# Kernel tuning notes

Hardware: AMD Instinct MI355X
Metric: run time of the kernel (lower is better)

Reference implementation:

```python
import jax, jax.numpy as jnp
import numpy as np

N_NODES = 49984   # 32 graphs x 1562 nodes
N_EDGES = 799744  # avg degree 16
DIM_IN = 64
WIDTH = 256
DEPTH = 3         # depth+1 = 4 GCNConv blocks
N_GRAPHS = 32
NODES_PER_GRAPH = 1562


def setup_inputs() -> dict:
    key = jax.random.key(0)
    ks = jax.random.split(key, 12)
    nb = DEPTH + 1
    s_f = 1.0 / np.sqrt(DIM_IN)
    s_g = 1.0 / np.sqrt(WIDTH)
    return {
        "x": jax.random.normal(ks[0], (N_NODES, DIM_IN), dtype=jnp.float32),
        "edge_index": jax.random.randint(ks[1], (2, N_EDGES), 0, N_NODES, dtype=jnp.int32),
        "center": jax.random.randint(ks[2], (N_GRAPHS,), 0, NODES_PER_GRAPH, dtype=jnp.int32),
        "ptr": jnp.arange(N_GRAPHS + 1, dtype=jnp.int32) * NODES_PER_GRAPH,
        # foot: Conv1d(dim_input, width, 1) == per-node linear
        "Wf": jax.random.uniform(ks[3], (WIDTH, DIM_IN), jnp.float32, -s_f, s_f),
        "bf": jax.random.uniform(ks[4], (WIDTH,), jnp.float32, -s_f, s_f),
        # stacked GCNConv params: weight [nb, width, width] (in->out), bias [nb, width]
        "Wg": jax.random.uniform(ks[5], (nb, WIDTH, WIDTH), jnp.float32, -s_g, s_g),
        "bg": jax.random.uniform(ks[6], (nb, WIDTH), jnp.float32, -s_g, s_g),
        # head: Conv1d(width, 7, 1)
        "Wh": jax.random.uniform(ks[7], (7, WIDTH), jnp.float32, -s_g, s_g),
        "bh": jax.random.uniform(ks[8], (7,), jnp.float32, -s_g, s_g),
    }


def reference(x, edge_index, center, ptr, Wf, bf, Wg, bg, Wh, bh):
    N = x.shape[0]
    # foot: 1x1 conv (per-node linear) + exact GELU; dropout = identity (eval)
    h = jax.nn.gelu(x @ Wf.T + bf, approximate=False)  # [N, W]

    # gcn_norm with self-loops (same for every layer since edges are static)
    loops = jnp.arange(N, dtype=edge_index.dtype)
    row = jnp.concatenate([edge_index[0], loops])  # source
    col = jnp.concatenate([edge_index[1], loops])  # target
    deg = jax.ops.segment_sum(jnp.ones_like(row, dtype=h.dtype), col, num_segments=N)
    dis = jnp.where(deg > 0, jax.lax.rsqrt(jnp.maximum(deg, 1.0)), 0.0)
    norm = dis[row] * dis[col]  # [E+N]

    for l in range(Wg.shape[0]):
        xl = h @ Wg[l]                                   # [N, W] linear transform
        msg = xl[row] * norm[:, None]                    # gather + edge scale
        agg = jax.ops.segment_sum(msg, col, num_segments=N) + bg[l]
        h = h + agg                                      # residual

    out = jax.nn.gelu(h, approximate=False) @ Wh.T + bh  # [N, 7]
    return out[center + ptr[:-1]]                        # [B, 7]
```

## Files before the change

kernel.cpp:

```cpp
#include <hip/hip_runtime.h>
#include <math.h>

#define WIDTH 256
typedef unsigned short u16;
typedef unsigned int u32;
typedef __attribute__((ext_vector_type(4))) float f32x4;
typedef __attribute__((ext_vector_type(8))) short bf16x8;

__device__ __forceinline__ float gelu_exact(float v) {
    return 0.5f * v * (1.0f + erff(v * 0.70710678118654752f));
}
__device__ __forceinline__ u16 f2b(float x) {
    u32 u = __builtin_bit_cast(u32, x);
    return (u16)((u + 0x7fffu + ((u >> 16) & 1u)) >> 16);
}
__device__ __forceinline__ float b2f_lo(u32 v) {
    return __builtin_bit_cast(float, v << 16);
}
__device__ __forceinline__ float b2f_hi(u32 v) {
    return __builtin_bit_cast(float, v & 0xffff0000u);
}
__device__ __forceinline__ float b2fu(u16 b) {
    return __builtin_bit_cast(float, ((u32)b) << 16);
}
__device__ __forceinline__ u32 pack2(float a, float b) {
    return (u32)f2b(a) | ((u32)f2b(b) << 16);
}

#define PREP_WG   (4 * 65536)
#define PREP_WF   (256 * 64)
__global__ void k_prep(const float* __restrict__ Wg, const float* __restrict__ Wf,
                       const float* __restrict__ x,
                       u16* __restrict__ WgT, u16* __restrict__ WfT,
                       u16* __restrict__ xb, int total8) {
    int idx = blockIdx.x * blockDim.x + threadIdx.x;
    if (idx < PREP_WG) {
        int l = idx >> 16;
        int k = (idx >> 8) & 255;
        int n = idx & 255;
        WgT[(size_t)l * 65536 + (size_t)n * 256 + k] = f2b(Wg[idx]);
    } else if (idx < PREP_WG + PREP_WF) {
        int j = idx - PREP_WG;
        WfT[j] = f2b(Wf[j]);
    } else if (idx < PREP_WG + PREP_WF + total8) {
        int i = idx - (PREP_WG + PREP_WF);
        const float4 v0 = *reinterpret_cast<const float4*>(&x[(size_t)i * 8]);
        const float4 v1 = *reinterpret_cast<const float4*>(&x[(size_t)i * 8 + 4]);
        uint4 o;
        o.x = pack2(v0.x, v0.y);
        o.y = pack2(v0.z, v0.w);
        o.z = pack2(v1.x, v1.y);
        o.w = pack2(v1.z, v1.w);
        *reinterpret_cast<uint4*>(&xb[(size_t)i * 8]) = o;
    }
}

__global__ void k_hist(const int* __restrict__ col, int* __restrict__ deg,
                       u16* __restrict__ rank, int E) {
    int i = blockIdx.x * blockDim.x + threadIdx.x;
    if (i < E) rank[i] = (u16)atomicAdd(&deg[col[i]], 1);
}

__global__ __launch_bounds__(256) void k_scan1(const int* __restrict__ deg, int* __restrict__ off,
                                               int* __restrict__ part, float* __restrict__ dis, int N) {
    __shared__ int buf[256];
    const int t = threadIdx.x;
    const int gid = blockIdx.x * 256 + t;
    const int v = (gid < N) ? deg[gid] : 0;
    if (gid < N) dis[gid] = rsqrtf(1.0f + (float)v);
    buf[t] = v;
    __syncthreads();
#pragma unroll
    for (int d = 1; d < 256; d <<= 1) {
        int add = (t >= d) ? buf[t - d] : 0;
        __syncthreads();
        buf[t] += add;
        __syncthreads();
    }
    if (gid < N) off[gid] = buf[t] - v;
    if (t == 255) part[blockIdx.x] = buf[255];
}

__global__ __launch_bounds__(256) void k_scan3(int* __restrict__ off, const int* __restrict__ part,
                                               int NB, int N, int E) {
    __shared__ int buf[256];
    const int t = threadIdx.x;
    int v = (t < NB) ? part[t] : 0;
    buf[t] = v;
    __syncthreads();
#pragma unroll
    for (int d = 1; d < 256; d <<= 1) {
        int add = (t >= d) ? buf[t - d] : 0;
        __syncthreads();
        buf[t] += add;
        __syncthreads();
    }
    const int base = (blockIdx.x == 0) ? 0 : buf[blockIdx.x - 1];
    const int gid = blockIdx.x * 256 + t;
    if (gid < N) off[gid] += base;
    if (gid == 0) off[N] = E;
}

__global__ void k_fill(const int* __restrict__ row, const int* __restrict__ col,
                       const u16* __restrict__ rank, const float* __restrict__ dis,
                       const int* __restrict__ off, u32* __restrict__ csr, int E) {
    int i = blockIdx.x * blockDim.x + threadIdx.x;
    if (i < E) {
        const int r = row[i];
        const int pos = off[col[i]] + (int)rank[i];
        csr[pos] = (u32)(u16)r | ((u32)f2b(dis[r]) << 16);
    }
}

__global__ void k_front(const int* __restrict__ center, const int* __restrict__ ptr,
                        const int* __restrict__ off, const u32* __restrict__ csr,
                        int* __restrict__ flags, int* __restrict__ list, int* __restrict__ cnt) {
    const int g = blockIdx.x;
    const int node = center[g] + ptr[g];
    const int t = threadIdx.x;
    const int e0 = off[node];
    const int e1 = off[node + 1];
    if (t == 0) {
        if (atomicExch(&flags[node], 1) == 0) list[atomicAdd(cnt, 1)] = node;
    }
    for (int e = e0 + t; e < e1; e += 256) {
        const int s = (int)(csr[e] & 0xffffu);
        if (atomicExch(&flags[s], 1) == 0) list[atomicAdd(cnt, 1)] = s;
    }
}

__global__ void k_front2(const int* __restrict__ off, const u32* __restrict__ csr,
                         const int* __restrict__ list1, const int* __restrict__ cnt1,
                         int* __restrict__ flags2, int* __restrict__ list2, int* __restrict__ cnt2) {
    const int n1 = cnt1[0];
    const int t = threadIdx.x;
    for (int idx = blockIdx.x; idx < n1; idx += gridDim.x) {
        const int node = list1[idx];
        if (t == 0) {
            if (atomicExch(&flags2[node], 1) == 0) list2[atomicAdd(cnt2, 1)] = node;
        }
        const int e0 = off[node];
        const int e1 = off[node + 1];
        for (int e = e0 + t; e < e1; e += 256) {
            const int s = (int)(csr[e] & 0xffffu);
            if (atomicExch(&flags2[s], 1) == 0) list2[atomicAdd(cnt2, 1)] = s;
        }
    }
}

template <int KDIM, bool FOOT>
__global__ __launch_bounds__(512) void k_gemm_mfma(const u16* __restrict__ A,
                                                   const u16* __restrict__ BT,
                                                   const float* __restrict__ bias,
                                                   u16* __restrict__ Cb,
                                                   float* __restrict__ Cf, int nrows) {
    __shared__ u16 As[128 * 64];
    __shared__ u16 Bs[256 * 64];

    const int tid = threadIdx.x;
    const int w = tid >> 6;
    const int l = tid & 63;
    const int m0 = blockIdx.x * 128;
    const int wr = w >> 2;
    const int wc = w & 3;

    const int lr = l >> 3;
    const int lc = l & 7;
    const int src_slot = lc ^ lr;

    f32x4 acc[4][4] = {};

#pragma unroll
    for (int ks = 0; ks < KDIM / 64; ++ks) {
        const int k0 = ks * 64;
#pragma unroll
        for (int i = 0; i < 2; ++i) {
            const u16* asrc = A + (size_t)(m0 + 16 * w + 8 * i + lr) * KDIM + k0 + src_slot * 8;
            __builtin_amdgcn_global_load_lds(
                (const __attribute__((address_space(1))) u32*)asrc,
                (__attribute__((address_space(3))) u32*)(As + (16 * w + 8 * i) * 64), 16, 0, 0);
        }
#pragma unroll
        for (int j = 0; j < 4; ++j) {
            const u16* bsrc = BT + (size_t)(32 * w + 8 * j + lr) * KDIM + k0 + src_slot * 8;
            __builtin_amdgcn_global_load_lds(
                (const __attribute__((address_space(1))) u32*)bsrc,
                (__attribute__((address_space(3))) u32*)(Bs + (32 * w + 8 * j) * 64), 16, 0, 0);
        }
        asm volatile("s_waitcnt vmcnt(0)" ::: "memory");
        __syncthreads();

        bf16x8 a[4][2], b[4][2];
#pragma unroll
        for (int fr = 0; fr < 4; ++fr) {
            const int row = 64 * wr + fr * 16 + (l & 15);
#pragma unroll
            for (int kk = 0; kk < 2; ++kk)
                a[fr][kk] = *reinterpret_cast<const bf16x8*>(
                    &As[row * 64 + ((kk * 4 + (l >> 4)) ^ (row & 7)) * 8]);
        }
#pragma unroll
        for (int fc = 0; fc < 4; ++fc) {
            const int row = 64 * wc + fc * 16 + (l & 15);
#pragma unroll
            for (int kk = 0; kk < 2; ++kk)
                b[fc][kk] = *reinterpret_cast<const bf16x8*>(
                    &Bs[row * 64 + ((kk * 4 + (l >> 4)) ^ (row & 7)) * 8]);
        }
#pragma unroll
        for (int fr = 0; fr < 4; ++fr)
#pragma unroll
            for (int fc = 0; fc < 4; ++fc) {
                acc[fr][fc] = __builtin_amdgcn_mfma_f32_16x16x32_bf16(a[fr][0], b[fc][0], acc[fr][fc], 0, 0, 0);
                acc[fr][fc] = __builtin_amdgcn_mfma_f32_16x16x32_bf16(a[fr][1], b[fc][1], acc[fr][fc], 0, 0, 0);
            }
        __syncthreads();
    }

    const int r0 = (l >> 4) * 4;
    const int ci = l & 15;
#pragma unroll
    for (int fr = 0; fr < 4; ++fr)
#pragma unroll
        for (int fc = 0; fc < 4; ++fc) {
            const int col = 64 * wc + fc * 16 + ci;
#pragma unroll
            for (int r = 0; r < 4; ++r) {
                const int row = m0 + 64 * wr + fr * 16 + r0 + r;
                if (row < nrows) {
                    const size_t p = (size_t)row * WIDTH + col;
                    if (FOOT) {
                        const float o = gelu_exact(acc[fr][fc][r] + bias[col]);
                        Cf[p] = o;
                        Cb[p] = f2b(o);
                    } else {
                        Cb[p] = f2b(acc[fr][fc][r]);
                    }
                }
            }
        }
}

#define EDGE_FMA(vv, dd_)                          \
    acc[0] = fmaf(dd_, b2f_lo(vv.x), acc[0]);      \
    acc[1] = fmaf(dd_, b2f_hi(vv.x), acc[1]);      \
    acc[2] = fmaf(dd_, b2f_lo(vv.y), acc[2]);      \
    acc[3] = fmaf(dd_, b2f_hi(vv.y), acc[3]);

__device__ __forceinline__ void agg_node_body(const int* __restrict__ off,
                                              const u32* __restrict__ csr,
                                              const float* __restrict__ dis,
                                              const u16* __restrict__ xlb,
                                              const float* __restrict__ bg,
                                              float* __restrict__ h,
                                              u16* __restrict__ hb,
                                              int node, int hl, int ch0) {
    const int c = ch0 + hl * 4;
    const int e0 = off[node];
    const int e1 = off[node + 1];
    const float di = dis[node];

    float acc[4];
    {
        const uint2 v = *reinterpret_cast<const uint2*>(&xlb[(size_t)node * WIDTH + c]);
        acc[0] = di * b2f_lo(v.x);
        acc[1] = di * b2f_hi(v.x);
        acc[2] = di * b2f_lo(v.y);
        acc[3] = di * b2f_hi(v.y);
    }

    for (int base = e0; base < e1; base += 32) {
        const int m = min(32, e1 - base);
        u32 ep = 0;
        if (hl < m) ep = csr[base + hl];
        int j = 0;
        for (; j + 8 <= m; j += 8) {
            uint2 vv[8];
            float dd[8];
#pragma unroll
            for (int q = 0; q < 8; ++q) {
                const u32 e = (u32)__shfl((int)ep, j + q, 32);
                dd[q] = b2f_hi(e);
                vv[q] = *reinterpret_cast<const uint2*>(&xlb[(size_t)(e & 0xffffu) * WIDTH + c]);
            }
#pragma unroll
            for (int q = 0; q < 8; ++q) { EDGE_FMA(vv[q], dd[q]) }
        }
        if (j + 4 <= m) {
            uint2 vv[4];
            float dd[4];
#pragma unroll
            for (int q = 0; q < 4; ++q) {
                const u32 e = (u32)__shfl((int)ep, j + q, 32);
                dd[q] = b2f_hi(e);
                vv[q] = *reinterpret_cast<const uint2*>(&xlb[(size_t)(e & 0xffffu) * WIDTH + c]);
            }
#pragma unroll
            for (int q = 0; q < 4; ++q) { EDGE_FMA(vv[q], dd[q]) }
            j += 4;
        }
        for (; j < m; ++j) {
            const u32 e = (u32)__shfl((int)ep, j, 32);
            const float dj = b2f_hi(e);
            const uint2 v = *reinterpret_cast<const uint2*>(&xlb[(size_t)(e & 0xffffu) * WIDTH + c]);
            EDGE_FMA(v, dj)
        }
    }

    const size_t p = (size_t)node * WIDTH + c;
    const float4 hv = *reinterpret_cast<const float4*>(&h[p]);
    const float4 bv = *reinterpret_cast<const float4*>(&bg[c]);
    const float o0 = hv.x + bv.x + di * acc[0];
    const float o1 = hv.y + bv.y + di * acc[1];
    const float o2 = hv.z + bv.z + di * acc[2];
    const float o3 = hv.w + bv.w + di * acc[3];
    float4 w0;
    w0.x = o0; w0.y = o1; w0.z = o2; w0.w = o3;
    *reinterpret_cast<float4*>(&h[p]) = w0;
    uint2 ob;
    ob.x = pack2(o0, o1);
    ob.y = pack2(o2, o3);
    *reinterpret_cast<uint2*>(&hb[p]) = ob;
}

__global__ __launch_bounds__(256) void k_agg(const int* __restrict__ off,
                                             const u32* __restrict__ csr,
                                             const float* __restrict__ dis,
                                             const u16* __restrict__ xlb,
                                             const float* __restrict__ bg,
                                             float* __restrict__ h,
                                             u16* __restrict__ hb, int nbh, int N) {
    int bh = blockIdx.x;
    int ch0 = 0;
    if (bh >= nbh) { ch0 = 128; bh -= nbh; }
    const int node = (bh * 256 + threadIdx.x) >> 5;
    if (node >= N) return;
    agg_node_body(off, csr, dis, xlb, bg, h, hb, node, threadIdx.x & 31, ch0);
}

__global__ __launch_bounds__(256) void k_agg_list(const int* __restrict__ off,
                                                  const u32* __restrict__ csr,
                                                  const float* __restrict__ dis,
                                                  const u16* __restrict__ xlb,
                                                  const float* __restrict__ bg,
                                                  float* __restrict__ h,
                                                  u16* __restrict__ hb,
                                                  const int* __restrict__ list,
                                                  const int* __restrict__ cnt) {
    const int nitems = cnt[0] * 2;
    const int hl = threadIdx.x & 31;
    const int stride = (gridDim.x * 256) >> 5;
    for (int item = (blockIdx.x * 256 + threadIdx.x) >> 5; item < nitems; item += stride) {
        const int node = list[item >> 1];
        const int ch0 = (item & 1) << 7;
        agg_node_body(off, csr, dis, xlb, bg, h, hb, node, hl, ch0);
    }
}
#undef EDGE_FMA

__global__ __launch_bounds__(256) void k_tail(const int* __restrict__ off,
                                              const u32* __restrict__ csr,
                                              const float* __restrict__ dis,
                                              const u16* __restrict__ hb,
                                              const float* __restrict__ h,
                                              const float* __restrict__ Wg3,
                                              const float* __restrict__ bg3,
                                              const float* __restrict__ Wh,
                                              const float* __restrict__ bh,
                                              const int* __restrict__ center,
                                              const int* __restrict__ ptr,
                                              float* __restrict__ out) {
    __shared__ float aggK[256];
    __shared__ u32 es[256];
    __shared__ float gs[256];
    const int g = blockIdx.x;
    const int t = threadIdx.x;
    const int node = center[g] + ptr[g];
    const int e0 = off[node];
    const int e1 = off[node + 1];
    const float di = dis[node];

    float acc = di * b2fu(hb[(size_t)node * WIDTH + t]);
    for (int base = e0; base < e1; base += 256) {
        const int m = min(256, e1 - base);
        if (t < m) es[t] = csr[base + t];
        __syncthreads();
        int j = 0;
        for (; j + 4 <= m; j += 4) {
            const u32 a0 = es[j + 0], a1 = es[j + 1], a2 = es[j + 2], a3 = es[j + 3];
            const float v0 = b2fu(hb[(size_t)(a0 & 0xffffu) * WIDTH + t]);
            const float v1 = b2fu(hb[(size_t)(a1 & 0xffffu) * WIDTH + t]);
            const float v2 = b2fu(hb[(size_t)(a2 & 0xffffu) * WIDTH + t]);
            const float v3 = b2fu(hb[(size_t)(a3 & 0xffffu) * WIDTH + t]);
            acc = fmaf(b2f_hi(a0), v0, acc);
            acc = fmaf(b2f_hi(a1), v1, acc);
            acc = fmaf(b2f_hi(a2), v2, acc);
            acc = fmaf(b2f_hi(a3), v3, acc);
        }
        for (; j < m; ++j) {
            const u32 a = es[j];
            acc = fmaf(b2f_hi(a), b2fu(hb[(size_t)(a & 0xffffu) * WIDTH + t]), acc);
        }
        __syncthreads();
    }
    aggK[t] = acc;
    __syncthreads();

    float mv = 0.0f;
#pragma unroll 8
    for (int k = 0; k < 256; ++k)
        mv = fmaf(aggK[k], Wg3[(size_t)k * 256 + t], mv);
    const float h4 = h[(size_t)node * WIDTH + t] + bg3[t] + di * mv;
    gs[t] = gelu_exact(h4);
    __syncthreads();
    if (t < 7) {
        float o = bh[t];
        for (int k = 0; k < 256; ++k)
            o = fmaf(gs[k], Wh[t * 256 + k], o);
        out[g * 7 + t] = o;
    }
}

extern "C" void kernel_launch(void* const* d_in, const int* in_sizes, int n_in,
                              void* d_out, int out_size, void* d_ws, size_t ws_size,
                              hipStream_t stream) {
    const float* x      = (const float*)d_in[0];
    const int*   ei     = (const int*)d_in[1];
    const int*   center = (const int*)d_in[2];
    const int*   ptr    = (const int*)d_in[3];
    const float* Wf     = (const float*)d_in[4];
    const float* bf     = (const float*)d_in[5];
    const float* Wg     = (const float*)d_in[6];
    const float* bg     = (const float*)d_in[7];
    const float* Wh     = (const float*)d_in[8];
    const float* bh     = (const float*)d_in[9];

    const int E = in_sizes[1] / 2;
    const int N = in_sizes[0] / 64;
    const int B = in_sizes[2];

    char* ws = (char*)d_ws;
    size_t o = 0;
    float* h       = (float*)(ws + o); o += (size_t)N * WIDTH * 4;
    u16*   hb      = (u16*)  (ws + o); o += (size_t)N * WIDTH * 2;
    u16*   xlb     = (u16*)  (ws + o); o += (size_t)N * WIDTH * 2;
    u16*   xb      = (u16*)  (ws + o); o += (size_t)N * 64 * 2;
    float* dis     = (float*)(ws + o); o += (size_t)N * 4;
    int*   deg     = (int*)  (ws + o); o += (size_t)N * 4;
    int*   off     = (int*)  (ws + o); o += (size_t)(N + 1) * 4;
    int*   part    = (int*)  (ws + o); o += 1024;
    u16*   rank    = (u16*)  (ws + o); o += (size_t)E * 2;
    u32*   csr     = (u32*)  (ws + o); o += (size_t)E * 4;
    u16*   WgT     = (u16*)  (ws + o); o += (size_t)4 * 65536 * 2;
    u16*   WfT     = (u16*)  (ws + o); o += (size_t)256 * 64 * 2;
    int*   flags   = (int*)  (ws + o); o += (size_t)N * 4;
    int*   flags2  = (int*)  (ws + o); o += (size_t)N * 4;
    int*   cnt     = (int*)  (ws + o); o += 128;
    int*   cnt2    = (int*)  (ws + o); o += 128;
    int*   list1   = (int*)  (ws + o); o += (size_t)N * 4;
    int*   list2   = (int*)  (ws + o); o += (size_t)N * 4;

    const int* rowv = ei;
    const int* colv = ei + E;

    const int nb = (N + 255) / 256;
    const int eb = (E + 255) / 256;

    hipMemsetAsync(deg, 0, (size_t)N * 4, stream);
    hipMemsetAsync(flags, 0, (size_t)N * 8 + 256, stream);
    const int total8 = N * 64 / 8;
    const int prep_threads = PREP_WG + PREP_WF + total8;
    k_prep<<<(prep_threads + 255) / 256, 256, 0, stream>>>(Wg, Wf, x, WgT, WfT, xb, total8);
    k_hist<<<eb, 256, 0, stream>>>(colv, deg, rank, E);
    k_scan1<<<nb, 256, 0, stream>>>(deg, off, part, dis, N);
    k_scan3<<<nb, 256, 0, stream>>>(off, part, nb, N, E);
    k_fill<<<eb, 256, 0, stream>>>(rowv, colv, rank, dis, off, csr, E);
    k_front<<<B, 256, 0, stream>>>(center, ptr, off, csr, flags, list1, cnt);
    k_front2<<<64, 256, 0, stream>>>(off, csr, list1, cnt, flags2, list2, cnt2);

    const int gb = (N + 127) / 128;
    k_gemm_mfma<64, true><<<gb, 512, 0, stream>>>(xb, WfT, bf, hb, h, N);

    const int nbh = N / 8;
    k_gemm_mfma<256, false><<<gb, 512, 0, stream>>>(hb, WgT, nullptr, xlb, nullptr, N);
    k_agg<<<2 * nbh, 256, 0, stream>>>(off, csr, dis, xlb, bg, h, hb, nbh, N);

    k_gemm_mfma<256, false><<<gb, 512, 0, stream>>>(hb, WgT + (size_t)1 * 65536, nullptr, xlb, nullptr, N);
    k_agg_list<<<1024, 256, 0, stream>>>(off, csr, dis, xlb, bg + (size_t)1 * WIDTH, h, hb, list2, cnt2);

    k_gemm_mfma<256, false><<<gb, 512, 0, stream>>>(hb, WgT + (size_t)2 * 65536, nullptr, xlb, nullptr, N);
    k_agg_list<<<256, 256, 0, stream>>>(off, csr, dis, xlb, bg + (size_t)2 * WIDTH, h, hb, list1, cnt);

    k_tail<<<B, 256, 0, stream>>>(off, csr, dis, hb, h,
                                  Wg + (size_t)3 * 65536, bg + (size_t)3 * WIDTH,
                                  Wh, bh, center, ptr, (float*)d_out);
}
```

Baseline: 273.3 us.

## Restrict layer-3 GEMM to gathered frontier rows and split degree histogram atomics

```diff
diff --git a/kernel.cpp b/kernel.cpp
--- a/kernel.cpp
+++ b/kernel.cpp
@@ -55,29 +55,42 @@
     }
 }
 
-__global__ void k_hist(const int* __restrict__ col, int* __restrict__ deg,
-                       u16* __restrict__ rank, int E) {
+__global__ void k_hist8(const int* __restrict__ col, int* __restrict__ deg8,
+                        u16* __restrict__ rank, int E, int N) {
     int i = blockIdx.x * blockDim.x + threadIdx.x;
-    if (i < E) rank[i] = (u16)atomicAdd(&deg[col[i]], 1);
-}
-
-__global__ __launch_bounds__(256) void k_scan1(const int* __restrict__ deg, int* __restrict__ off,
-                                               int* __restrict__ part, float* __restrict__ dis, int N) {
+    if (i < E) {
+        const int c = blockIdx.x & 7;
+        rank[i] = (u16)atomicAdd(&deg8[(size_t)c * N + col[i]], 1);
+    }
+}
+
+__global__ __launch_bounds__(256) void k_scan1(const int* __restrict__ deg8, int* __restrict__ off,
+                                               int* __restrict__ part, float* __restrict__ dis,
+                                               u16* __restrict__ base8, int N) {
     __shared__ int buf[256];
     const int t = threadIdx.x;
     const int gid = blockIdx.x * 256 + t;
-    const int v = (gid < N) ? deg[gid] : 0;
-    if (gid < N) dis[gid] = rsqrtf(1.0f + (float)v);
-    buf[t] = v;
+    int d = 0;
+    if (gid < N) {
+        int run = 0;
+#pragma unroll
+        for (int c = 0; c < 8; ++c) {
+            base8[(size_t)c * N + gid] = (u16)run;
+            run += deg8[(size_t)c * N + gid];
+        }
+        d = run;
+        dis[gid] = rsqrtf(1.0f + (float)run);
+    }
+    buf[t] = d;
     __syncthreads();
 #pragma unroll
-    for (int d = 1; d < 256; d <<= 1) {
-        int add = (t >= d) ? buf[t - d] : 0;
+    for (int dd = 1; dd < 256; dd <<= 1) {
+        int add = (t >= dd) ? buf[t - dd] : 0;
         __syncthreads();
         buf[t] += add;
         __syncthreads();
     }
-    if (gid < N) off[gid] = buf[t] - v;
+    if (gid < N) off[gid] = buf[t] - d;
     if (t == 255) part[blockIdx.x] = buf[255];
 }
 
@@ -102,12 +115,15 @@
 }
 
 __global__ void k_fill(const int* __restrict__ row, const int* __restrict__ col,
-                       const u16* __restrict__ rank, const float* __restrict__ dis,
-                       const int* __restrict__ off, u32* __restrict__ csr, int E) {
+                       const u16* __restrict__ rank, const u16* __restrict__ base8,
+                       const float* __restrict__ dis,
+                       const int* __restrict__ off, u32* __restrict__ csr, int E, int N) {
     int i = blockIdx.x * blockDim.x + threadIdx.x;
     if (i < E) {
+        const int c = blockIdx.x & 7;
         const int r = row[i];
-        const int pos = off[col[i]] + (int)rank[i];
+        const int cc = col[i];
+        const int pos = off[cc] + (int)base8[(size_t)c * N + cc] + (int)rank[i];
         csr[pos] = (u32)(u16)r | ((u32)f2b(dis[r]) << 16);
     }
 }
@@ -239,6 +255,94 @@
                 }
             }
         }
+}
+
+__global__ __launch_bounds__(512) void k_gemm_gather(const u16* __restrict__ A,
+                                                     const u16* __restrict__ BT,
+                                                     u16* __restrict__ Cb,
+                                                     const int* __restrict__ list,
+                                                     const int* __restrict__ cnt) {
+    __shared__ u16 As[128 * 64];
+    __shared__ u16 Bs[256 * 64];
+
+    const int nrows = cnt[0];
+    const int tid = threadIdx.x;
+    const int w = tid >> 6;
+    const int l = tid & 63;
+    const int wr = w >> 2;
+    const int wc = w & 3;
+
+    const int lr = l >> 3;
+    const int lc = l & 7;
+    const int src_slot = lc ^ lr;
+
+    for (int m0 = blockIdx.x * 128; m0 < nrows; m0 += gridDim.x * 128) {
+        f32x4 acc[4][4] = {};
+
+#pragma unroll
+        for (int ks = 0; ks < 4; ++ks) {
+            const int k0 = ks * 64;
+#pragma unroll
+            for (int i = 0; i < 2; ++i) {
+                int ridx = m0 + 16 * w + 8 * i + lr;
+                ridx = min(ridx, nrows - 1);
+                const u16* asrc = A + (size_t)list[ridx] * WIDTH + k0 + src_slot * 8;
+                __builtin_amdgcn_global_load_lds(
+                    (const __attribute__((address_space(1))) u32*)asrc,
+                    (__attribute__((address_space(3))) u32*)(As + (16 * w + 8 * i) * 64), 16, 0, 0);
+            }
+#pragma unroll
+            for (int j = 0; j < 4; ++j) {
+                const u16* bsrc = BT + (size_t)(32 * w + 8 * j + lr) * WIDTH + k0 + src_slot * 8;
+                __builtin_amdgcn_global_load_lds(
+                    (const __attribute__((address_space(1))) u32*)bsrc,
+                    (__attribute__((address_space(3))) u32*)(Bs + (32 * w + 8 * j) * 64), 16, 0, 0);
+            }
+            asm volatile("s_waitcnt vmcnt(0)" ::: "memory");
+            __syncthreads();
+
+            bf16x8 a[4][2], b[4][2];
+#pragma unroll
+            for (int fr = 0; fr < 4; ++fr) {
+                const int row = 64 * wr + fr * 16 + (l & 15);
+#pragma unroll
+                for (int kk = 0; kk < 2; ++kk)
+                    a[fr][kk] = *reinterpret_cast<const bf16x8*>(
+                        &As[row * 64 + ((kk * 4 + (l >> 4)) ^ (row & 7)) * 8]);
+            }
+#pragma unroll
+            for (int fc = 0; fc < 4; ++fc) {
+                const int row = 64 * wc + fc * 16 + (l & 15);
+#pragma unroll
+                for (int kk = 0; kk < 2; ++kk)
+                    b[fc][kk] = *reinterpret_cast<const bf16x8*>(
+                        &Bs[row * 64 + ((kk * 4 + (l >> 4)) ^ (row & 7)) * 8]);
+            }
+#pragma unroll
+            for (int fr = 0; fr < 4; ++fr)
+#pragma unroll
+                for (int fc = 0; fc < 4; ++fc) {
+                    acc[fr][fc] = __builtin_amdgcn_mfma_f32_16x16x32_bf16(a[fr][0], b[fc][0], acc[fr][fc], 0, 0, 0);
+                    acc[fr][fc] = __builtin_amdgcn_mfma_f32_16x16x32_bf16(a[fr][1], b[fc][1], acc[fr][fc], 0, 0, 0);
+                }
+            __syncthreads();
+        }
+
+        const int r0 = (l >> 4) * 4;
+        const int ci = l & 15;
+#pragma unroll
+        for (int fr = 0; fr < 4; ++fr)
+#pragma unroll
+            for (int fc = 0; fc < 4; ++fc) {
+                const int col = 64 * wc + fc * 16 + ci;
+#pragma unroll
+                for (int r = 0; r < 4; ++r) {
+                    const int row = m0 + 64 * wr + fr * 16 + r0 + r;
+                    if (row < nrows)
+                        Cb[(size_t)list[row] * WIDTH + col] = f2b(acc[fr][fc][r]);
+                }
+            }
+    }
 }
 
 #define EDGE_FMA(vv, dd_)                          \
@@ -446,7 +550,8 @@
     u16*   xlb     = (u16*)  (ws + o); o += (size_t)N * WIDTH * 2;
     u16*   xb      = (u16*)  (ws + o); o += (size_t)N * 64 * 2;
     float* dis     = (float*)(ws + o); o += (size_t)N * 4;
-    int*   deg     = (int*)  (ws + o); o += (size_t)N * 4;
+    int*   deg8    = (int*)  (ws + o); o += (size_t)N * 8 * 4;
+    u16*   base8   = (u16*)  (ws + o); o += (size_t)N * 8 * 2;
     int*   off     = (int*)  (ws + o); o += (size_t)(N + 1) * 4;
     int*   part    = (int*)  (ws + o); o += 1024;
     u16*   rank    = (u16*)  (ws + o); o += (size_t)E * 2;
@@ -466,15 +571,15 @@
     const int nb = (N + 255) / 256;
     const int eb = (E + 255) / 256;
 
-    hipMemsetAsync(deg, 0, (size_t)N * 4, stream);
+    hipMemsetAsync(deg8, 0, (size_t)N * 8 * 4, stream);
     hipMemsetAsync(flags, 0, (size_t)N * 8 + 256, stream);
     const int total8 = N * 64 / 8;
     const int prep_threads = PREP_WG + PREP_WF + total8;
     k_prep<<<(prep_threads + 255) / 256, 256, 0, stream>>>(Wg, Wf, x, WgT, WfT, xb, total8);
-    k_hist<<<eb, 256, 0, stream>>>(colv, deg, rank, E);
-    k_scan1<<<nb, 256, 0, stream>>>(deg, off, part, dis, N);
+    k_hist8<<<eb, 256, 0, stream>>>(colv, deg8, rank, E, N);
+    k_scan1<<<nb, 256, 0, stream>>>(deg8, off, part, dis, base8, N);
     k_scan3<<<nb, 256, 0, stream>>>(off, part, nb, N, E);
-    k_fill<<<eb, 256, 0, stream>>>(rowv, colv, rank, dis, off, csr, E);
+    k_fill<<<eb, 256, 0, stream>>>(rowv, colv, rank, base8, dis, off, csr, E, N);
     k_front<<<B, 256, 0, stream>>>(center, ptr, off, csr, flags, list1, cnt);
     k_front2<<<64, 256, 0, stream>>>(off, csr, list1, cnt, flags2, list2, cnt2);
 
@@ -488,7 +593,7 @@
     k_gemm_mfma<256, false><<<gb, 512, 0, stream>>>(hb, WgT + (size_t)1 * 65536, nullptr, xlb, nullptr, N);
     k_agg_list<<<1024, 256, 0, stream>>>(off, csr, dis, xlb, bg + (size_t)1 * WIDTH, h, hb, list2, cnt2);
 
-    k_gemm_mfma<256, false><<<gb, 512, 0, stream>>>(hb, WgT + (size_t)2 * 65536, nullptr, xlb, nullptr, N);
+    k_gemm_gather<<<128, 512, 0, stream>>>(hb, WgT + (size_t)2 * 65536, xlb, list2, cnt2);
     k_agg_list<<<256, 256, 0, stream>>>(off, csr, dis, xlb, bg + (size_t)2 * WIDTH, h, hb, list1, cnt);
 
     k_tail<<<B, 256, 0, stream>>>(off, csr, dis, hb, h,
```

Result: no change. 274.9 us (+0.6%).
